# Optimization experiments

Measured on AMD Instinct MI355X. Metric: run time of the kernel, lower is better.

## Reference

```python
import jax, jax.numpy as jnp
import numpy as np

N_USER, N_VIDEO, N_PUB, N_TAG = 200000, 100000, 20000, 5000
EMB = 128
HALF = EMB // 2
LAYER_NUM = 3


def setup_inputs() -> dict:
    key = jax.random.key(0)
    ks = jax.random.split(key, 20)
    inp = {
        "user_emb": jax.random.normal(ks[0], (N_USER, EMB), jnp.float32),
        "video_emb": jax.random.normal(ks[1], (N_VIDEO, EMB), jnp.float32),
        "publisher_emb": jax.random.normal(ks[2], (N_PUB, EMB), jnp.float32),
        "tag_emb": jax.random.normal(ks[3], (N_TAG, EMB), jnp.float32),
    }
    # (name, E, n_src, n_dst)
    rels = [
        ("uv", 1500000, N_USER, N_VIDEO),
        ("vu", 1500000, N_VIDEO, N_USER),
        ("up", 800000, N_USER, N_PUB),
        ("pu", 800000, N_PUB, N_USER),
        ("vt", 800000, N_VIDEO, N_TAG),
        ("tv", 800000, N_TAG, N_VIDEO),
        ("pt", 400000, N_PUB, N_TAG),
        ("tp", 400000, N_TAG, N_PUB),
    ]
    for i, (name, E, ns, nd) in enumerate(rels):
        inp[name + "_src"] = jax.random.randint(ks[4 + 2 * i], (E,), 0, ns, jnp.int32)
        inp[name + "_dst"] = jax.random.randint(ks[5 + 2 * i], (E,), 0, nd, jnp.int32)
    return inp


def _seg_mean(feat, src, dst, num_dst):
    # copy_u + mean: gather half-dim src features, segment-mean onto dst.
    msg = feat[src]                                             # [E, HALF]
    s = jax.ops.segment_sum(msg, dst, num_segments=num_dst)     # [num_dst, HALF]
    deg = jax.ops.segment_sum(jnp.ones_like(dst, dtype=feat.dtype), dst,
                              num_segments=num_dst)
    return s / jnp.maximum(deg, 1.0)[:, None]  # zero-in-degree nodes -> 0 (DGL behavior)


def reference(user_emb, video_emb, publisher_emb, tag_emb,
              uv_src, uv_dst, vu_src, vu_dst,
              up_src, up_dst, pu_src, pu_dst,
              vt_src, vt_dst, tv_src, tv_dst,
              pt_src, pt_dst, tp_src, tp_dst):

    def layer(u, v, p, t):
        # user dst: [vu, pu]; video dst: [uv, tv]; publisher dst: [up, tp]; tag dst: [vt, pt]
        vu = _seg_mean(v[:, :HALF], vu_src, vu_dst, N_USER)
        pu = _seg_mean(p[:, :HALF], pu_src, pu_dst, N_USER)
        uv = _seg_mean(u[:, :HALF], uv_src, uv_dst, N_VIDEO)
        tv = _seg_mean(t[:, :HALF], tv_src, tv_dst, N_VIDEO)
        up = _seg_mean(u[:, HALF:], up_src, up_dst, N_PUB)
        tp = _seg_mean(t[:, HALF:], tp_src, tp_dst, N_PUB)
        vt = _seg_mean(v[:, HALF:], vt_src, vt_dst, N_TAG)
        pt = _seg_mean(p[:, HALF:], pt_src, pt_dst, N_TAG)
        return (jnp.concatenate([vu, pu], axis=1),
                jnp.concatenate([uv, tv], axis=1),
                jnp.concatenate([up, tp], axis=1),
                jnp.concatenate([vt, pt], axis=1))

    pu_, pv_, pp_, pt_ = user_emb, video_emb, publisher_emb, tag_emb
    u, v, p, t = user_emb, video_emb, publisher_emb, tag_emb
    for i in range(LAYER_NUM):
        u, v, p, t = layer(u, v, p, t)
        w = 1.0 / (i + 2)
        pu_ = pu_ + u * w
        pv_ = pv_ + v * w
        pp_ = pp_ + p * w
        pt_ = pt_ + t * w
    return (pu_, pv_, pp_, pt_)
```

## Files before the change

### kernel.cpp

```cpp
#include <hip/hip_runtime.h>
#include <stdint.h>

#define EMB 128
#define PCAP 12288
#define SCAP 13312

static constexpr int N_USER = 200000, N_VIDEO = 100000, N_PUB = 20000, N_TAG = 5000;
static constexpr int ROW_U = 0, ROW_V = 200000, ROW_P = 300000, ROW_T = 320000;
static constexpr int ROWS = 325000;
static constexpr int TOTAL_E = 7000000;
static constexpr int TOTAL_GROUPS = 650000;
static constexpr int TILE = 8192;
static constexpr int SORT_MAX = TOTAL_E + 7 * TOTAL_GROUPS;

using f32x4 = __attribute__((ext_vector_type(4))) float;
using u32x4 = __attribute__((ext_vector_type(4))) unsigned int;
using u32x2 = __attribute__((ext_vector_type(2))) unsigned int;

__device__ inline unsigned bf16_rne(float f) {
  unsigned u = __float_as_uint(f);
  return (u + 0x7fffu + ((u >> 16) & 1u)) >> 16;
}
__device__ inline unsigned pack_bf16x2(float lo, float hi) {
  return bf16_rne(lo) | (bf16_rne(hi) << 16);
}

__device__ inline unsigned fp8enc(float f) {
  unsigned b = __float_as_uint(f);
  unsigned s = (b >> 24) & 0x80u;
  unsigned ae = b & 0x7FFFFFFFu;
  unsigned r = ae + 0x7FFFFu + ((ae >> 20) & 1u);
  unsigned e = r >> 23;
  if (e < 121u) {
    float av = __uint_as_float(ae);
    unsigned m = (unsigned)__builtin_rintf(av * 512.0f);
    return s | m;
  }
  return s | ((e - 120u) << 3) | ((r >> 20) & 7u);
}
#if __has_builtin(__builtin_amdgcn_cvt_f32_fp8)
#define DEC4(w, x0, x1, x2, x3) \
  x0 += __builtin_amdgcn_cvt_f32_fp8((int)(w), 0); \
  x1 += __builtin_amdgcn_cvt_f32_fp8((int)(w), 1); \
  x2 += __builtin_amdgcn_cvt_f32_fp8((int)(w), 2); \
  x3 += __builtin_amdgcn_cvt_f32_fp8((int)(w), 3);
#else
__device__ inline float fp8dec(unsigned b) {
  unsigned s = (b & 0x80u) << 24;
  unsigned e = (b >> 3) & 0xFu;
  unsigned m = b & 7u;
  if (e == 0) { float f = (float)m * 0.001953125f; return s ? -f : f; }
  return __uint_as_float(s | ((e + 120u) << 23) | (m << 20));
}
#define DEC4(w, x0, x1, x2, x3) \
  x0 += fp8dec((w) & 0xffu); x1 += fp8dec(((w) >> 8) & 0xffu); \
  x2 += fp8dec(((w) >> 16) & 0xffu); x3 += fp8dec(((w) >> 24) & 0xffu);
#endif

struct SortDesc {
  int tcum[9];
  int bcum[9];
  int gcum[8];
  int E[8];
  int n_dst[8];
  int wshift[8];
  int zrow[8];
  const int* esrc[8];
  const int* edst[8];
};

struct AggrDesc {
  int cum[9];
  int src_base[8];
  int src_col[8];
  int dst_base[8];
  int dst_col[8];
  const float* demb[8];
};

__global__ __launch_bounds__(256) void part_kernel(SortDesc d, unsigned* __restrict__ pairs,
                                                   int* __restrict__ cursors) {
  __shared__ int cnt[256];
  __shared__ int lcur[256];
  int blk = blockIdx.x;
  int r = 0;
#pragma unroll
  for (int k = 1; k < 8; ++k) if (blk >= d.tcum[k]) r = k;
  int base = (blk - d.tcum[r]) * TILE;
  int n = min(TILE, d.E[r] - base);
  const int* __restrict__ esrc = d.esrc[r];
  const int* __restrict__ edst = d.edst[r];
  int tid = threadIdx.x;
  int B = d.bcum[r + 1] - d.bcum[r];
  int sh = d.wshift[r];
  int msk = (1 << sh) - 1;
  int bb = d.bcum[r];
  if (tid < B) cnt[tid] = 0;
  __syncthreads();
  for (int i = tid; i < n; i += 256)
    atomicAdd(&cnt[edst[base + i] >> sh], 1);
  __syncthreads();
  if (tid < B) {
    int c = cnt[tid];
    lcur[tid] = c ? atomicAdd(&cursors[bb + tid], c) : 0;
  }
  __syncthreads();
  for (int i = tid; i < n; i += 256) {
    int dv = edst[base + i];
    int sv = esrc[base + i];
    int b = dv >> sh;
    int pos = atomicAdd(&lcur[b], 1);
    if (pos < PCAP)
      pairs[(size_t)(bb + b) * PCAP + pos] = ((unsigned)(dv & msk) << 18) | (unsigned)sv;
  }
}

__global__ __launch_bounds__(256) void build_kernel(SortDesc d, const unsigned* __restrict__ pairs,
                                                    const int* __restrict__ cursors,
                                                    int* __restrict__ gcounter,
                                                    int* __restrict__ sorted,
                                                    int* __restrict__ Beg, int* __restrict__ Deg) {
  __shared__ int cnt[1024];
  __shared__ int poff[1025];
  __shared__ int stage[SCAP];
  __shared__ int wsums[4];
  __shared__ int sh_gbase;
  int bucket = blockIdx.x;
  int r = 0;
#pragma unroll
  for (int k = 1; k < 8; ++k) if (bucket >= d.bcum[k]) r = k;
  int bl = bucket - d.bcum[r];
  int sh = d.wshift[r];
  int first = bl << sh;
  int Wa = min(1 << sh, d.n_dst[r] - first);
  int zr = d.zrow[r];
  int tid = threadIdx.x;
  int n_b = min(cursors[bucket], PCAP);
  const unsigned* __restrict__ bp = pairs + (size_t)bucket * PCAP;

  for (int i = tid; i < 1024; i += 256) cnt[i] = 0;
  __syncthreads();
  for (int i = tid; i < n_b; i += 256)
    atomicAdd(&cnt[bp[i] >> 18], 1);
  __syncthreads();

  int t4 = tid * 4;
  int c0 = cnt[t4], c1 = cnt[t4 + 1], c2 = cnt[t4 + 2], c3 = cnt[t4 + 3];
  int p0 = (c0 + 7) & ~7, p1 = (c1 + 7) & ~7, p2 = (c2 + 7) & ~7, p3 = (c3 + 7) & ~7;
  int s = p0 + p1 + p2 + p3;
  int lane = tid & 63, wv = tid >> 6;
  int v = s;
#pragma unroll
  for (int dd = 1; dd < 64; dd <<= 1) {
    int t = __shfl_up(v, dd);
    if (lane >= dd) v += t;
  }
  if (lane == 63) wsums[wv] = v;
  __syncthreads();
  if (tid == 0) {
    int run = 0;
#pragma unroll
    for (int k = 0; k < 4; ++k) { int t = wsums[k]; wsums[k] = run; run += t; }
  }
  __syncthreads();
  int ex = wsums[wv] + (v - s);
  if (tid == 255) {
    int tot = ex + s;
    sh_gbase = atomicAdd(gcounter, tot);
    poff[1024] = min(tot, SCAP);
  }
  __syncthreads();
  int gbase = sh_gbase;
  int o0 = ex, o1 = ex + p0, o2 = o1 + p1, o3 = o2 + p2;
  cnt[t4] = o0; cnt[t4 + 1] = o1; cnt[t4 + 2] = o2; cnt[t4 + 3] = o3;
  poff[t4] = o0; poff[t4 + 1] = o1; poff[t4 + 2] = o2; poff[t4 + 3] = o3;
  int g0 = d.gcum[r] + first + t4;
  if (t4 + 0 < Wa) { Beg[g0 + 0] = gbase + o0; Deg[g0 + 0] = c0; }
  if (t4 + 1 < Wa) { Beg[g0 + 1] = gbase + o1; Deg[g0 + 1] = c1; }
  if (t4 + 2 < Wa) { Beg[g0 + 2] = gbase + o2; Deg[g0 + 2] = c2; }
  if (t4 + 3 < Wa) { Beg[g0 + 3] = gbase + o3; Deg[g0 + 3] = c3; }
  __syncthreads();

  for (int i = tid; i < n_b; i += 256) {
    unsigned pr = bp[i];
    int pos = atomicAdd(&cnt[pr >> 18], 1);
    if (pos < SCAP) stage[pos] = (int)(pr & 0x3FFFFu);
  }
  __syncthreads();
#pragma unroll
  for (int jj = 0; jj < 4; ++jj) {
    int j = t4 + jj;
    int end_ = min((j < 1023) ? poff[j + 1] : poff[1024], SCAP);
    for (int k = cnt[j]; k < end_; ++k) stage[k] = zr;
  }
  __syncthreads();

  int tot = poff[1024];
  for (int i = tid; i < tot; i += 256)
    sorted[gbase + i] = stage[i];
}

__global__ void convert_kernel(const float* __restrict__ u, const float* __restrict__ v,
                               const float* __restrict__ p, const float* __restrict__ t,
                               uint16_t* __restrict__ featA, uint16_t* __restrict__ featB) {
  int idx = blockIdx.x * blockDim.x + threadIdx.x;
  const int total8 = (ROWS + 1) * EMB / 8;
  if (idx >= total8) return;
  int flat = idx * 8;
  int row = flat >> 7;
  if (row == ROWS) {
    uint4 z = {0u, 0u, 0u, 0u};
    *(uint4*)(featA + flat) = z;
    *(uint4*)(featB + flat) = z;
    return;
  }
  int col = flat & 127;
  const float* s;
  if (row < ROW_V)      s = u + (size_t)row * EMB + col;
  else if (row < ROW_P) s = v + (size_t)(row - ROW_V) * EMB + col;
  else if (row < ROW_T) s = p + (size_t)(row - ROW_P) * EMB + col;
  else                  s = t + (size_t)(row - ROW_T) * EMB + col;
  float4 f0 = *(const float4*)s;
  float4 f1 = *((const float4*)s + 1);
  uint4 o;
  o.x = pack_bf16x2(f0.x, f0.y);
  o.y = pack_bf16x2(f0.z, f0.w);
  o.z = pack_bf16x2(f1.x, f1.y);
  o.w = pack_bf16x2(f1.z, f1.w);
  *(uint4*)(featA + flat) = o;
}

#define ACC(q) \
  a0 += __uint_as_float((q).x << 16); a1 += __uint_as_float((q).x & 0xffff0000u); \
  a2 += __uint_as_float((q).y << 16); a3 += __uint_as_float((q).y & 0xffff0000u); \
  a4 += __uint_as_float((q).z << 16); a5 += __uint_as_float((q).z & 0xffff0000u); \
  a6 += __uint_as_float((q).w << 16); a7 += __uint_as_float((q).w & 0xffff0000u);

#define ACC8(qq) \
  DEC4((qq).x, a0, a1, a2, a3); DEC4((qq).y, a4, a5, a6, a7);

template<int MODE>
__global__ __launch_bounds__(256) void aggr_kernel(AggrDesc d,
    const uint16_t* __restrict__ gsrc_bf, const unsigned char* __restrict__ gsrc_f8,
    uint16_t* __restrict__ dst_bf, unsigned char* __restrict__ dst_f8,
    const uint16_t* __restrict__ f1_bf, float* __restrict__ out,
    const int* __restrict__ sorted, const int* __restrict__ Beg,
    const int* __restrict__ Deg) {
  if (MODE == 1 && blockIdx.x == 0 && threadIdx.x < 16) {
    uint2 z = {0u, 0u};
    *(uint2*)(dst_f8 + (size_t)ROWS * EMB + threadIdx.x * 8) = z;
  }
  int g = blockIdx.x * 32 + (threadIdx.x >> 3);
  if (g >= TOTAL_GROUPS) return;
  int lane = threadIdx.x & 7;
  int r = 0;
#pragma unroll
  for (int k = 1; k < 8; ++k) if (g >= d.cum[k]) r = k;
  int n = g - d.cum[r];
  int beg = Beg[g], dg = Deg[g];
  float recip = 1.0f / (float)(dg > 0 ? dg : 1);
  const uint16_t* __restrict__ sb16 =
      gsrc_bf ? gsrc_bf + (size_t)d.src_base[r] * EMB + d.src_col[r] + lane * 8 : nullptr;
  const unsigned char* __restrict__ sb8 =
      gsrc_f8 ? gsrc_f8 + (size_t)d.src_base[r] * EMB + d.src_col[r] + lane * 8 : nullptr;
  float a0 = 0.f, a1 = 0.f, a2 = 0.f, a3 = 0.f, a4 = 0.f, a5 = 0.f, a6 = 0.f, a7 = 0.f;
  int nchunk = (dg + 7) >> 3;
  const int* ep = sorted + beg;
  int4 iA0 = {0,0,0,0}, iA1 = {0,0,0,0};
  if (nchunk > 0) { iA0 = *(const int4*)ep; iA1 = *(const int4*)(ep + 4); }
  for (int c = 0; c < nchunk; ++c) {
    int4 iB0 = {0,0,0,0}, iB1 = {0,0,0,0};
    if (c + 1 < nchunk) { iB0 = *(const int4*)(ep + 8); iB1 = *(const int4*)(ep + 12); }
    if (MODE < 2) {
      uint4 q0 = *(const uint4*)(sb16 + (size_t)iA0.x * EMB);
      uint4 q1 = *(const uint4*)(sb16 + (size_t)iA0.y * EMB);
      uint4 q2 = *(const uint4*)(sb16 + (size_t)iA0.z * EMB);
      uint4 q3 = *(const uint4*)(sb16 + (size_t)iA0.w * EMB);
      uint4 q4 = *(const uint4*)(sb16 + (size_t)iA1.x * EMB);
      uint4 q5 = *(const uint4*)(sb16 + (size_t)iA1.y * EMB);
      uint4 q6 = *(const uint4*)(sb16 + (size_t)iA1.z * EMB);
      uint4 q7 = *(const uint4*)(sb16 + (size_t)iA1.w * EMB);
      __builtin_amdgcn_sched_barrier(0);
      ACC(q0); ACC(q1); ACC(q2); ACC(q3);
      ACC(q4); ACC(q5); ACC(q6); ACC(q7);
    } else {
      uint2 q0 = *(const uint2*)(sb8 + (size_t)iA0.x * EMB);
      uint2 q1 = *(const uint2*)(sb8 + (size_t)iA0.y * EMB);
      uint2 q2 = *(const uint2*)(sb8 + (size_t)iA0.z * EMB);
      uint2 q3 = *(const uint2*)(sb8 + (size_t)iA0.w * EMB);
      uint2 q4 = *(const uint2*)(sb8 + (size_t)iA1.x * EMB);
      uint2 q5 = *(const uint2*)(sb8 + (size_t)iA1.y * EMB);
      uint2 q6 = *(const uint2*)(sb8 + (size_t)iA1.z * EMB);
      uint2 q7 = *(const uint2*)(sb8 + (size_t)iA1.w * EMB);
      __builtin_amdgcn_sched_barrier(0);
      ACC8(q0); ACC8(q1); ACC8(q2); ACC8(q3);
      ACC8(q4); ACC8(q5); ACC8(q6); ACC8(q7);
    }
    iA0 = iB0; iA1 = iB1; ep += 8;
  }
  a0 *= recip; a1 *= recip; a2 *= recip; a3 *= recip;
  a4 *= recip; a5 *= recip; a6 *= recip; a7 *= recip;

  int col = d.dst_col[r] + lane * 8;
  size_t dpos = (size_t)(d.dst_base[r] + n) * EMB + col;

  if (MODE == 0) {
    u32x4 ov;
    ov.x = pack_bf16x2(a0, a1);
    ov.y = pack_bf16x2(a2, a3);
    ov.z = pack_bf16x2(a4, a5);
    ov.w = pack_bf16x2(a6, a7);
    __builtin_nontemporal_store(ov, (u32x4*)(dst_bf + dpos));
    return;
  }
  if (MODE == 1) {
    u32x2 ov;
    ov.x = fp8enc(a0) | (fp8enc(a1) << 8) | (fp8enc(a2) << 16) | (fp8enc(a3) << 24);
    ov.y = fp8enc(a4) | (fp8enc(a5) << 8) | (fp8enc(a6) << 16) | (fp8enc(a7) << 24);
    __builtin_nontemporal_store(ov, (u32x2*)(dst_f8 + dpos));
    return;
  }

  u32x4 q1 = __builtin_nontemporal_load((const u32x4*)(f1_bf + dpos));
  u32x2 qf = __builtin_nontemporal_load((const u32x2*)(gsrc_f8 + dpos));
  float g0 = 0.f, g1 = 0.f, g2 = 0.f, g3 = 0.f, g4 = 0.f, g5 = 0.f, g6 = 0.f, g7 = 0.f;
  DEC4(qf.x, g0, g1, g2, g3);
  DEC4(qf.y, g4, g5, g6, g7);
  const f32x4* de = (const f32x4*)(d.demb[r] + (size_t)n * EMB + col);
  f32x4 v0 = __builtin_nontemporal_load(de);
  f32x4 v1 = __builtin_nontemporal_load(de + 1);
  const float w1 = 0.5f, w2 = 1.0f / 3.0f, w3 = 0.25f;
  v0.x += w1 * __uint_as_float(q1.x << 16)         + w2 * g0 + w3 * a0;
  v0.y += w1 * __uint_as_float(q1.x & 0xffff0000u) + w2 * g1 + w3 * a1;
  v0.z += w1 * __uint_as_float(q1.y << 16)         + w2 * g2 + w3 * a2;
  v0.w += w1 * __uint_as_float(q1.y & 0xffff0000u) + w2 * g3 + w3 * a3;
  v1.x += w1 * __uint_as_float(q1.z << 16)         + w2 * g4 + w3 * a4;
  v1.y += w1 * __uint_as_float(q1.z & 0xffff0000u) + w2 * g5 + w3 * a5;
  v1.z += w1 * __uint_as_float(q1.w << 16)         + w2 * g6 + w3 * a6;
  v1.w += w1 * __uint_as_float(q1.w & 0xffff0000u) + w2 * g7 + w3 * a7;
  __builtin_nontemporal_store(v0, (f32x4*)(out + dpos));
  __builtin_nontemporal_store(v1, (f32x4*)(out + dpos) + 1);
}

extern "C" void kernel_launch(void* const* d_in, const int* in_sizes, int n_in,
                              void* d_out, int out_size, void* d_ws, size_t ws_size,
                              hipStream_t stream) {
  const float* emb_u = (const float*)d_in[0];
  const float* emb_v = (const float*)d_in[1];
  const float* emb_p = (const float*)d_in[2];
  const float* emb_t = (const float*)d_in[3];

  struct RelInfo { int si, di, E, n_dst, src_base, src_col, dst_base, dst_col, wshift; };
  const RelInfo rels[8] = {
    {12, 13,  800000, N_TAG,   ROW_V, 64, ROW_T,  0,  5},
    {16, 17,  400000, N_TAG,   ROW_P, 64, ROW_T, 64,  5},
    { 8,  9,  800000, N_PUB,   ROW_U, 64, ROW_P,  0,  7},
    {18, 19,  400000, N_PUB,   ROW_T, 64, ROW_P, 64,  7},
    { 4,  5, 1500000, N_VIDEO, ROW_U,  0, ROW_V,  0,  9},
    {14, 15,  800000, N_VIDEO, ROW_T,  0, ROW_V, 64,  9},
    { 6,  7, 1500000, N_USER,  ROW_V,  0, ROW_U,  0, 10},
    {10, 11,  800000, N_USER,  ROW_P,  0, ROW_U, 64, 10},
  };
  const float* dembs[8] = {emb_t, emb_t, emb_p, emb_p, emb_v, emb_v, emb_u, emb_u};

  char* ws = (char*)d_ws;
  size_t cursor = 0;
  auto take = [&](size_t bytes) -> char* {
    char* p = ws + cursor;
    cursor = (cursor + bytes + 255) & ~(size_t)255;
    return p;
  };
  uint16_t* featA = (uint16_t*)take((size_t)(ROWS + 1) * EMB * 2);
  uint16_t* featB = (uint16_t*)take((size_t)(ROWS + 1) * EMB * 2);
  int* sorted = (int*)take((size_t)SORT_MAX * 4);
  int* Beg    = (int*)take((size_t)TOTAL_GROUPS * 4);
  int* Deg    = (int*)take((size_t)TOTAL_GROUPS * 4);
  unsigned* pairs = (unsigned*)d_ws;
  unsigned char* f2fp8 = (unsigned char*)featA;

  SortDesc sd;
  AggrDesc ad;
  int tacc = 0, bacc = 0, gacc = 0;
  for (int r = 0; r < 8; ++r) {
    int n_dst = rels[r].n_dst;
    sd.tcum[r] = tacc; tacc += (rels[r].E + TILE - 1) / TILE;
    sd.bcum[r] = bacc; bacc += (n_dst + (1 << rels[r].wshift) - 1) >> rels[r].wshift;
    sd.gcum[r] = gacc;
    sd.E[r] = rels[r].E;
    sd.n_dst[r] = n_dst;
    sd.wshift[r] = rels[r].wshift;
    sd.zrow[r] = ROWS - rels[r].src_base;
    sd.esrc[r] = (const int*)d_in[rels[r].si];
    sd.edst[r] = (const int*)d_in[rels[r].di];

    ad.cum[r] = gacc;
    ad.src_base[r] = rels[r].src_base;
    ad.src_col[r] = rels[r].src_col;
    ad.dst_base[r] = rels[r].dst_base;
    ad.dst_col[r] = rels[r].dst_col;
    ad.demb[r] = dembs[r];
    gacc += n_dst;
  }
  sd.tcum[8] = tacc;
  sd.bcum[8] = bacc;
  ad.cum[8] = gacc;

  int* cursors  = (int*)take((size_t)bacc * 4 + 4);
  int* gcounter = cursors + bacc;

  hipMemsetAsync(cursors, 0, (size_t)(bacc + 1) * 4, stream);
  part_kernel<<<tacc, 256, 0, stream>>>(sd, pairs, cursors);
  build_kernel<<<bacc, 256, 0, stream>>>(sd, pairs, cursors, gcounter, sorted, Beg, Deg);

  convert_kernel<<<((ROWS + 1) * EMB / 8 + 255) / 256, 256, 0, stream>>>(
      emb_u, emb_v, emb_p, emb_t, featA, featB);

  float* out = (float*)d_out;
  const int aggr_blocks = (TOTAL_GROUPS + 31) / 32;
  aggr_kernel<0><<<aggr_blocks, 256, 0, stream>>>(ad, featA, nullptr, featB, nullptr,
                                                  nullptr, nullptr, sorted, Beg, Deg);
  aggr_kernel<1><<<aggr_blocks, 256, 0, stream>>>(ad, featB, nullptr, nullptr, f2fp8,
                                                  nullptr, nullptr, sorted, Beg, Deg);
  aggr_kernel<2><<<aggr_blocks, 256, 0, stream>>>(ad, nullptr, f2fp8, nullptr, nullptr,
                                                  featB, out, sorted, Beg, Deg);
}
```

Measured before the change: 606.0 us.

## Gather layer-2 sources from fp8 copy and read bf16 embeddings in final pass

```diff
diff --git a/kernel.cpp b/kernel.cpp
--- a/kernel.cpp
+++ b/kernel.cpp
@@ -202,7 +202,8 @@
 
 __global__ void convert_kernel(const float* __restrict__ u, const float* __restrict__ v,
                                const float* __restrict__ p, const float* __restrict__ t,
-                               uint16_t* __restrict__ featA, uint16_t* __restrict__ featB) {
+                               uint16_t* __restrict__ featA, uint16_t* __restrict__ featB,
+                               unsigned char* __restrict__ f1f8) {
   int idx = blockIdx.x * blockDim.x + threadIdx.x;
   const int total8 = (ROWS + 1) * EMB / 8;
   if (idx >= total8) return;
@@ -212,6 +213,7 @@
     uint4 z = {0u, 0u, 0u, 0u};
     *(uint4*)(featA + flat) = z;
     *(uint4*)(featB + flat) = z;
+    if (f1f8) { uint2 z2 = {0u, 0u}; *(uint2*)(f1f8 + flat) = z2; }
     return;
   }
   int col = flat & 127;
@@ -239,14 +241,15 @@
 #define ACC8(qq) \
   DEC4((qq).x, a0, a1, a2, a3); DEC4((qq).y, a4, a5, a6, a7);
 
-template<int MODE>
+template<int M>
 __global__ __launch_bounds__(256) void aggr_kernel(AggrDesc d,
     const uint16_t* __restrict__ gsrc_bf, const unsigned char* __restrict__ gsrc_f8,
     uint16_t* __restrict__ dst_bf, unsigned char* __restrict__ dst_f8,
-    const uint16_t* __restrict__ f1_bf, float* __restrict__ out,
+    const uint16_t* __restrict__ f1_bf, const uint16_t* __restrict__ demb_bf,
+    float* __restrict__ out,
     const int* __restrict__ sorted, const int* __restrict__ Beg,
     const int* __restrict__ Deg) {
-  if (MODE == 1 && blockIdx.x == 0 && threadIdx.x < 16) {
+  if ((M == 1 || M == 3) && blockIdx.x == 0 && threadIdx.x < 16) {
     uint2 z = {0u, 0u};
     *(uint2*)(dst_f8 + (size_t)ROWS * EMB + threadIdx.x * 8) = z;
   }
@@ -259,10 +262,11 @@
   int n = g - d.cum[r];
   int beg = Beg[g], dg = Deg[g];
   float recip = 1.0f / (float)(dg > 0 ? dg : 1);
+  constexpr bool GB = (M == 0 || M == 3 || M == 4);
   const uint16_t* __restrict__ sb16 =
-      gsrc_bf ? gsrc_bf + (size_t)d.src_base[r] * EMB + d.src_col[r] + lane * 8 : nullptr;
+      GB ? gsrc_bf + (size_t)d.src_base[r] * EMB + d.src_col[r] + lane * 8 : nullptr;
   const unsigned char* __restrict__ sb8 =
-      gsrc_f8 ? gsrc_f8 + (size_t)d.src_base[r] * EMB + d.src_col[r] + lane * 8 : nullptr;
+      !GB ? gsrc_f8 + (size_t)d.src_base[r] * EMB + d.src_col[r] + lane * 8 : nullptr;
   float a0 = 0.f, a1 = 0.f, a2 = 0.f, a3 = 0.f, a4 = 0.f, a5 = 0.f, a6 = 0.f, a7 = 0.f;
   int nchunk = (dg + 7) >> 3;
   const int* ep = sorted + beg;
@@ -271,7 +275,7 @@
   for (int c = 0; c < nchunk; ++c) {
     int4 iB0 = {0,0,0,0}, iB1 = {0,0,0,0};
     if (c + 1 < nchunk) { iB0 = *(const int4*)(ep + 8); iB1 = *(const int4*)(ep + 12); }
-    if (MODE < 2) {
+    if (GB) {
       uint4 q0 = *(const uint4*)(sb16 + (size_t)iA0.x * EMB);
       uint4 q1 = *(const uint4*)(sb16 + (size_t)iA0.y * EMB);
       uint4 q2 = *(const uint4*)(sb16 + (size_t)iA0.z * EMB);
@@ -304,16 +308,22 @@
   int col = d.dst_col[r] + lane * 8;
   size_t dpos = (size_t)(d.dst_base[r] + n) * EMB + col;
 
-  if (MODE == 0) {
+  if (M == 0 || M == 4) {
     u32x4 ov;
     ov.x = pack_bf16x2(a0, a1);
     ov.y = pack_bf16x2(a2, a3);
     ov.z = pack_bf16x2(a4, a5);
     ov.w = pack_bf16x2(a6, a7);
     __builtin_nontemporal_store(ov, (u32x4*)(dst_bf + dpos));
+    if (M == 4) {
+      u32x2 o8;
+      o8.x = fp8enc(a0) | (fp8enc(a1) << 8) | (fp8enc(a2) << 16) | (fp8enc(a3) << 24);
+      o8.y = fp8enc(a4) | (fp8enc(a5) << 8) | (fp8enc(a6) << 16) | (fp8enc(a7) << 24);
+      __builtin_nontemporal_store(o8, (u32x2*)(dst_f8 + dpos));
+    }
     return;
   }
-  if (MODE == 1) {
+  if (M == 1 || M == 3) {
     u32x2 ov;
     ov.x = fp8enc(a0) | (fp8enc(a1) << 8) | (fp8enc(a2) << 16) | (fp8enc(a3) << 24);
     ov.y = fp8enc(a4) | (fp8enc(a5) << 8) | (fp8enc(a6) << 16) | (fp8enc(a7) << 24);
@@ -326,9 +336,18 @@
   float g0 = 0.f, g1 = 0.f, g2 = 0.f, g3 = 0.f, g4 = 0.f, g5 = 0.f, g6 = 0.f, g7 = 0.f;
   DEC4(qf.x, g0, g1, g2, g3);
   DEC4(qf.y, g4, g5, g6, g7);
-  const f32x4* de = (const f32x4*)(d.demb[r] + (size_t)n * EMB + col);
-  f32x4 v0 = __builtin_nontemporal_load(de);
-  f32x4 v1 = __builtin_nontemporal_load(de + 1);
+  f32x4 v0, v1;
+  if (demb_bf) {
+    u32x4 qe = __builtin_nontemporal_load((const u32x4*)(demb_bf + dpos));
+    v0.x = __uint_as_float(qe.x << 16); v0.y = __uint_as_float(qe.x & 0xffff0000u);
+    v0.z = __uint_as_float(qe.y << 16); v0.w = __uint_as_float(qe.y & 0xffff0000u);
+    v1.x = __uint_as_float(qe.z << 16); v1.y = __uint_as_float(qe.z & 0xffff0000u);
+    v1.z = __uint_as_float(qe.w << 16); v1.w = __uint_as_float(qe.w & 0xffff0000u);
+  } else {
+    const f32x4* de = (const f32x4*)(d.demb[r] + (size_t)n * EMB + col);
+    v0 = __builtin_nontemporal_load(de);
+    v1 = __builtin_nontemporal_load(de + 1);
+  }
   const float w1 = 0.5f, w2 = 1.0f / 3.0f, w3 = 0.25f;
   v0.x += w1 * __uint_as_float(q1.x << 16)         + w2 * g0 + w3 * a0;
   v0.y += w1 * __uint_as_float(q1.x & 0xffff0000u) + w2 * g1 + w3 * a1;
@@ -376,7 +395,6 @@
   int* Beg    = (int*)take((size_t)TOTAL_GROUPS * 4);
   int* Deg    = (int*)take((size_t)TOTAL_GROUPS * 4);
   unsigned* pairs = (unsigned*)d_ws;
-  unsigned char* f2fp8 = (unsigned char*)featA;
 
   SortDesc sd;
   AggrDesc ad;
@@ -408,19 +426,41 @@
   int* cursors  = (int*)take((size_t)bacc * 4 + 4);
   int* gcounter = cursors + bacc;
 
+  const size_t f8bytes = (size_t)(ROWS + 1) * EMB;
+  size_t base_need = cursor;
+  unsigned char* f1fp8 = nullptr;
+  unsigned char* f2fp8 = (unsigned char*)featA;
+  bool use_fp8_l1 = false;
+  const uint16_t* demb_bf = nullptr;
+  if (ws_size >= base_need + f8bytes + 256) {
+    f1fp8 = (unsigned char*)take(f8bytes);
+    use_fp8_l1 = true;
+    if (ws_size >= cursor + f8bytes + 256) {
+      f2fp8 = (unsigned char*)take(f8bytes);
+      demb_bf = featA;
+    }
+  }
+
   hipMemsetAsync(cursors, 0, (size_t)(bacc + 1) * 4, stream);
   part_kernel<<<tacc, 256, 0, stream>>>(sd, pairs, cursors);
   build_kernel<<<bacc, 256, 0, stream>>>(sd, pairs, cursors, gcounter, sorted, Beg, Deg);
 
   convert_kernel<<<((ROWS + 1) * EMB / 8 + 255) / 256, 256, 0, stream>>>(
-      emb_u, emb_v, emb_p, emb_t, featA, featB);
+      emb_u, emb_v, emb_p, emb_t, featA, featB, f1fp8);
 
   float* out = (float*)d_out;
   const int aggr_blocks = (TOTAL_GROUPS + 31) / 32;
-  aggr_kernel<0><<<aggr_blocks, 256, 0, stream>>>(ad, featA, nullptr, featB, nullptr,
-                                                  nullptr, nullptr, sorted, Beg, Deg);
-  aggr_kernel<1><<<aggr_blocks, 256, 0, stream>>>(ad, featB, nullptr, nullptr, f2fp8,
-                                                  nullptr, nullptr, sorted, Beg, Deg);
+  if (use_fp8_l1) {
+    aggr_kernel<4><<<aggr_blocks, 256, 0, stream>>>(ad, featA, nullptr, featB, f1fp8,
+                                                    nullptr, nullptr, nullptr, sorted, Beg, Deg);
+    aggr_kernel<1><<<aggr_blocks, 256, 0, stream>>>(ad, nullptr, f1fp8, nullptr, f2fp8,
+                                                    nullptr, nullptr, nullptr, sorted, Beg, Deg);
+  } else {
+    aggr_kernel<0><<<aggr_blocks, 256, 0, stream>>>(ad, featA, nullptr, featB, nullptr,
+                                                    nullptr, nullptr, nullptr, sorted, Beg, Deg);
+    aggr_kernel<3><<<aggr_blocks, 256, 0, stream>>>(ad, featB, nullptr, nullptr, f2fp8,
+                                                    nullptr, nullptr, nullptr, sorted, Beg, Deg);
+  }
   aggr_kernel<2><<<aggr_blocks, 256, 0, stream>>>(ad, nullptr, f2fp8, nullptr, nullptr,
-                                                  featB, out, sorted, Beg, Deg);
-}
+                                                  featB, demb_bf, out, sorted, Beg, Deg);
+}
```

Result: no change. 599.6 us (-1.1%).
